# Kernel tuning notes

Measured on AMD Instinct MI355X. Metric: run time of the kernel, lower is better.

## Reference

```python
import jax, jax.numpy as jnp
import numpy as np

TAU = 0.1
K = 60.0
CHUNK = 64
B = 1024


def setup_inputs() -> dict:
    key = jax.random.key(0)
    k1, k2, k3, k4 = jax.random.split(key, 4)
    s_v = jax.random.normal(k1, (B, B), jnp.float32)
    s_l = jax.random.normal(k2, (B, B), jnp.float32)
    # class-label based positive/negative masks (typical metric-learning batch)
    labels = jax.random.randint(k3, (B,), 0, B // 8)
    pos_mask = labels[:, None] == labels[None, :]
    neg_mask = ~pos_mask
    w_v = jax.random.uniform(k4, (B, B), jnp.float32)
    w_l = 1.0 - w_v
    return dict(s_v=s_v, s_l=s_l, pos_mask=pos_mask, neg_mask=neg_mask, w_v=w_v, w_l=w_l)


def _soft_ranks(sim, pos_f, neg_f, tau=TAU, chunk=CHUNK):
    """Row-chunked differentiable soft ranks. sim/pos_f/neg_f: [B, B] float."""
    b = sim.shape[0]
    nc = b // chunk  # B divisible by chunk

    def body(args):
        cs, cp, cn = args                                   # [chunk, B] each
        # sig[c, k, j] = sigmoid((s_ck - s_cj) / tau)
        sig = jax.nn.sigmoid((cs[:, :, None] - cs[:, None, :]) / tau)
        rank_pos = 1.0 + jnp.einsum('ckj,ck->cj', sig, cn)  # count negatives above
        rank_neg = 1.0 + jnp.einsum('ckj,ck->cj', sig, cp)  # count positives above
        return rank_pos * cp + rank_neg * cn

    args = (sim.reshape(nc, chunk, b), pos_f.reshape(nc, chunk, b), neg_f.reshape(nc, chunk, b))
    return jax.lax.map(jax.checkpoint(body), args).reshape(b, b)


def reference(s_v, s_l, pos_mask, neg_mask, w_v, w_l):
    pos_f = pos_mask.astype(s_v.dtype)
    neg_f = neg_mask.astype(s_v.dtype)
    rank_v = _soft_ranks(s_v, pos_f, neg_f)
    rank_l = _soft_ranks(s_l, pos_f, neg_f)
    S_hat = (K + 1.0) * (w_v / (K + rank_v) + w_l / (K + rank_l))
    return S_hat
```

## Files before the change

### kernel.cpp

```cpp
#include <hip/hip_runtime.h>


#define NB 1024
#define CEXP 14.426950408889634f
#define SCL  0.000030517578125f
#define NBUK 128
#define BUK0 4.3f
#define BUKW 14.883720930f
#define DBUK 4
#define CHSZ 128
#define NJOB 32
#define MAXPOS 64
#define ECLMP 1e17f

typedef __attribute__((ext_vector_type(2))) float f32x2;
typedef __attribute__((ext_vector_type(2))) int   i32x2;

__device__ __forceinline__ f32x2 pk_fma(f32x2 a, f32x2 b, f32x2 c) {
    f32x2 d;
    asm("v_pk_fma_f32 %0, %1, %2, %3" : "=v"(d) : "v"(a), "v"(b), "v"(c));
    return d;
}
__device__ __forceinline__ f32x2 pk_mul(f32x2 a, f32x2 b) {
    f32x2 d;
    asm("v_pk_mul_f32 %0, %1, %2" : "=v"(d) : "v"(a), "v"(b));
    return d;
}
__device__ __forceinline__ f32x2 pk_add(f32x2 a, f32x2 b) {
    f32x2 d;
    asm("v_pk_add_f32 %0, %1, %2" : "=v"(d) : "v"(a), "v"(b));
    return d;
}
__device__ __forceinline__ f32x2 pk_fma_sat_lo(f32x2 es, f32x2 rp, f32x2 scl) {
    f32x2 d;
    asm("v_pk_fma_f32 %0, %1, %2, %3 op_sel_hi:[1,0,1] clamp"
        : "=v"(d) : "v"(es), "v"(rp), "v"(scl));
    return d;
}
__device__ __forceinline__ f32x2 pk_fma_sat_hi(f32x2 es, f32x2 rp, f32x2 scl) {
    f32x2 d;
    asm("v_pk_fma_f32 %0, %1, %2, %3 op_sel:[0,1,0] clamp"
        : "=v"(d) : "v"(es), "v"(rp), "v"(scl));
    return d;
}

#define PKTREE(L2q, Es2, A2, SCL2, TWO2, M1C)                      \
    {                                                              \
        const f32x2 P0 = (L2q)[0], P1 = (L2q)[1];                  \
        const f32x2 P2 = (L2q)[2], P3 = (L2q)[3];                  \
        const f32x2 y1 = pk_fma_sat_lo((Es2), P0, (SCL2));         \
        const f32x2 y2 = pk_fma_sat_hi((Es2), P0, (SCL2));         \
        const f32x2 y3 = pk_fma_sat_lo((Es2), P1, (SCL2));         \
        const f32x2 y4 = pk_fma_sat_hi((Es2), P1, (SCL2));         \
        const f32x2 y5 = pk_fma_sat_lo((Es2), P2, (SCL2));         \
        const f32x2 y6 = pk_fma_sat_hi((Es2), P2, (SCL2));         \
        const f32x2 y7 = pk_fma_sat_lo((Es2), P3, (SCL2));         \
        const f32x2 y8 = pk_fma_sat_hi((Es2), P3, (SCL2));         \
        const f32x2 p12 = pk_mul(y1, y2), p34 = pk_mul(y3, y4);    \
        const f32x2 p56 = pk_mul(y5, y6), p78 = pk_mul(y7, y8);    \
        const f32x2 s12 = pk_add(y1, y2), s34 = pk_add(y3, y4);    \
        const f32x2 s56 = pk_add(y5, y6), s78 = pk_add(y7, y8);    \
        const f32x2 q1 = pk_mul(p12, p34), q2 = pk_mul(p56, p78);  \
        const f32x2 n1 = pk_fma(s12, p34, pk_mul(s34, p12));       \
        const f32x2 n2 = pk_fma(s56, p78, pk_mul(s78, p56));       \
        const f32x2 num = pk_fma(n1, q2, pk_mul(n2, q1));          \
        const f32x2 den = pk_mul(q1, q2);                          \
        const i32x2 bi = 0x7EF311C3 - __builtin_bit_cast(i32x2, den); \
        f32x2 rr = __builtin_bit_cast(f32x2, bi);                  \
        const f32x2 dn = pk_mul(den, (M1C));                       \
        rr = pk_mul(rr, pk_fma(dn, rr, (TWO2)));                   \
        rr = pk_mul(rr, pk_fma(dn, rr, (TWO2)));                   \
        (A2) = pk_fma(num, rr, (A2));                              \
    }

__global__ __launch_bounds__(512) void drank_kernel(
    const float* __restrict__ s_v, const float* __restrict__ s_l,
    const unsigned char* __restrict__ pos_m,
    const unsigned char* __restrict__ neg_m,
    const float* __restrict__ w_v, const float* __restrict__ w_l,
    float* __restrict__ out)
{
    __shared__ __align__(16) float listRv[NB], listRl[NB];
    __shared__ unsigned char bktv[NB], bktl[NB];
    __shared__ unsigned short invv[NB], invl[NB];
    __shared__ float  sAv1[NB], sAv2[NB];
    __shared__ float  sAl1[NB], sAl2[NB];
    __shared__ int    offv[NBUK + 1], offl[NBUK + 1];
    __shared__ int    curv[NBUK], curl[NBUK];
    __shared__ float  SRv[129], SEv[129];
    __shared__ float  SR2v[129], SE2v[129];
    __shared__ float  SRl[129], SEl[129];
    __shared__ float  SR2l[129], SE2l[129];
    __shared__ float2 posR[MAXPOS];
    __shared__ int    npos_s, jobCtr;

    const int c = blockIdx.x;
    const int t = threadIdx.x;
    const long row = (long)c * NB;

    if (t < NBUK) { curv[t] = 0; curl[t] = 0; }
    if (t == 0) { npos_s = 0; jobCtr = 0; }
    __syncthreads();

    const unsigned int W =
        ((const unsigned int*)pos_m)[0] ^ ((const unsigned int*)neg_m)[0];
    const int mode = (W == 0x01010101u) ? 0 : ((W == 0x3f800000u) ? 2 : 1);

    const int j0 = t * 2;
    const float2 sjv = *(const float2*)(s_v + row + j0);
    const float2 sjl = *(const float2*)(s_l + row + j0);
    const float svu[2] = {sjv.x, sjv.y};
    const float slu[2] = {sjl.x, sjl.y};

    float Rv[2], Rl[2], Ev[2], El[2];
    int ibv[2], ibl[2];
    #pragma unroll
    for (int u = 0; u < 2; ++u) {
        Rv[u] = __builtin_amdgcn_exp2f(-svu[u] * CEXP);
        Rl[u] = __builtin_amdgcn_exp2f(-slu[u] * CEXP);
        Ev[u] = __builtin_amdgcn_exp2f(svu[u] * CEXP);
        El[u] = __builtin_amdgcn_exp2f(slu[u] * CEXP);
        ibv[u] = max(0, min(NBUK - 1, (int)((svu[u] + BUK0) * BUKW)));
        ibl[u] = max(0, min(NBUK - 1, (int)((slu[u] + BUK0) * BUKW)));
        atomicAdd(&curv[ibv[u]], 1);
        atomicAdd(&curl[ibl[u]], 1);
    }

    bool pj[2];
    if (mode == 0) {
        const unsigned short b = ((const unsigned short*)pos_m)[(row >> 1) + t];
        pj[0] = (b & 0x00ffu) != 0; pj[1] = (b & 0xff00u) != 0;
    } else if (mode == 2) {
        const float2 p = *(const float2*)((const float*)pos_m + row + j0);
        pj[0] = p.x != 0.f; pj[1] = p.y != 0.f;
    } else {
        const int2 p = *(const int2*)((const int*)pos_m + row + j0);
        pj[0] = p.x != 0; pj[1] = p.y != 0;
    }
    #pragma unroll
    for (int u = 0; u < 2; ++u) {
        if (pj[u]) {
            const int idx = atomicAdd(&npos_s, 1);
            if (idx < MAXPOS) posR[idx] = make_float2(Rv[u], Rl[u]);
        }
    }
    __syncthreads();

    if (t < 128) {
        const int m = t >> 6, l = t & 63;
        int* cnt = m ? curl : curv;
        int* off = m ? offl : offv;
        const int c0 = cnt[2 * l], c1 = cnt[2 * l + 1];
        int s = c0 + c1;
        #pragma unroll
        for (int d = 1; d < 64; d <<= 1) {
            const int y = __shfl_up(s, d, 64);
            if (l >= d) s += y;
        }
        const int excl = s - c0 - c1;
        off[2 * l] = excl;     off[2 * l + 1] = excl + c0;
        cnt[2 * l] = excl;     cnt[2 * l + 1] = excl + c0;
        if (l == 63) off[NBUK] = s;
    }
    __syncthreads();

    #pragma unroll
    for (int u = 0; u < 2; ++u) {
        const int pv = atomicAdd(&curv[ibv[u]], 1);
        listRv[pv] = Rv[u];
        bktv[pv]   = (unsigned char)ibv[u];
        invv[j0 + u] = (unsigned short)pv;
        const int pl = atomicAdd(&curl[ibl[u]], 1);
        listRl[pl] = Rl[u];
        bktl[pl]   = (unsigned char)ibl[u];
        invl[j0 + u] = (unsigned short)pl;
    }
    __syncthreads();

    {
        const int wid = t >> 6, l = t & 63;
        const int m   = (wid >> 1) & 1;
        const int fE  = wid & 1;
        const int sq  = wid >> 2;
        const float4* L4 = (const float4*)(m ? listRl : listRv);
        float* arr;
        switch (wid) {
            case 0: arr = SRv;  break;  case 1: arr = SEv;  break;
            case 2: arr = SRl;  break;  case 3: arr = SEl;  break;
            case 4: arr = SR2v; break;  case 5: arr = SE2v; break;
            case 6: arr = SR2l; break;  default: arr = SE2l; break;
        }
        const int o0 = fE ? (2 * l) : (127 - 2 * l);
        const int o1 = fE ? (2 * l + 1) : (126 - 2 * l);
        float s01[2];
        #pragma unroll
        for (int q = 0; q < 2; ++q) {
            const int o = q ? o1 : o0;
            const float4 a = L4[2 * o], b = L4[2 * o + 1];
            float x[8] = {a.x, a.y, a.z, a.w, b.x, b.y, b.z, b.w};
            float acc = 0.f;
            #pragma unroll
            for (int i = 0; i < 8; ++i) {
                const float v = fE ? __builtin_amdgcn_rcpf(x[i]) : x[i];
                if (sq) { const float vc = fminf(v, ECLMP); acc += vc * vc; }
                else    { acc += v; }
            }
            s01[q] = acc;
        }
        float s = s01[0] + s01[1];
        #pragma unroll
        for (int d = 1; d < 64; d <<= 1) {
            const float y = __shfl_up(s, d, 64);
            if (l >= d) s += y;
        }
        if (fE) {
            const float excl = s - s01[0] - s01[1];
            arr[o0] = excl;  arr[o1] = excl + s01[0];
            if (l == 63) arr[128] = s;
        } else {
            arr[o1] = s;  arr[o0] = s - s01[1];
            if (l == 0) arr[128] = 0.f;
        }
    }
    __syncthreads();

    static const unsigned char CORD[8] = {3, 4, 2, 5, 1, 6, 0, 7};
    const int lane = t & 63;
    const f32x2 SCL2 = {SCL, SCL};
    const f32x2 TWO2 = {2.0f, 2.0f};
    const f32x2 M1C  = {-1.0f, -1.0f};

    for (;;) {
        int jid0 = 0;
        if (lane == 0) jid0 = atomicAdd(&jobCtr, 1);
        const int jid = __builtin_amdgcn_readfirstlane(jid0);
        if (jid >= NJOB) break;
        const int ch = CORD[jid >> 2];
        const int m  = (jid >> 1) & 1;
        const int h  = jid & 1;

        const float* LR  = m ? listRl : listRv;
        const unsigned char* BK = m ? bktl : bktv;
        const int*   off = m ? offl : offv;
        float*       SA  = h ? (m ? sAl2 : sAv2) : (m ? sAl1 : sAv1);
        const float* SR  = m ? SRl : SRv;
        const float* SE  = m ? SEl : SEv;
        const float* SR2 = m ? SR2l : SR2v;
        const float* SE2 = m ? SE2l : SE2v;
        const f32x2* L2  = (const f32x2*)LR;

        const int p0 = ch * CHSZ + 2 * lane;
        const float2 R2 = *(const float2*)(LR + p0);
        const float Ex = __builtin_amdgcn_rcpf(R2.x);
        const float Ey = __builtin_amdgcn_rcpf(R2.y);
        const f32x2 Es2 = {SCL * Ex, SCL * Ey};

        const int bs = (int)BK[ch * CHSZ];
        const int be = (int)BK[ch * CHSZ + CHSZ - 1];
        const int lo0 = off[max(0, bs - DBUK)] & ~7;
        const int hi0 = (off[min(NBUK - 1, be + DBUK) + 1] + 7) & ~7;
        const int mid = ((lo0 + hi0) >> 1) & ~7;
        const int lo = h ? mid : lo0;
        const int hi = h ? hi0 : mid;

        f32x2 A2 = {0.f, 0.f};
        #pragma unroll 2
        for (int p = lo; p < hi; p += 8) {
            const f32x2* L2q = L2 + (p >> 1);
            PKTREE(L2q, Es2, A2, SCL2, TWO2, M1C);
        }
        float cx, cy;
        if (h) {
            const float sr = SR[hi0 >> 3], sr2 = SR2[hi0 >> 3];
            const float Exc = fminf(Ex, ECLMP), Eyc = fminf(Ey, ECLMP);
            cx = fmaf(Exc * Exc, sr2, (float)(NB - hi0) - Ex * sr);
            cy = fmaf(Eyc * Eyc, sr2, (float)(NB - hi0) - Ey * sr);
        } else {
            const float se = SE[lo0 >> 3], se2 = SE2[lo0 >> 3];
            const float Rxc = fminf(R2.x, ECLMP), Ryc = fminf(R2.y, ECLMP);
            cx = fmaf(-(Rxc * Rxc), se2, R2.x * se);
            cy = fmaf(-(Ryc * Ryc), se2, R2.y * se);
        }
        float2 r;
        r.x = fmaf(A2.x, SCL, cx);
        r.y = fmaf(A2.y, SCL, cy);
        *(float2*)(SA + p0) = r;
    }

    float sPv[2] = {0.f, 0.f};
    float sPl[2] = {0.f, 0.f};
    const int np = min(npos_s, MAXPOS);
    for (int i = 0; i < np; ++i) {
        const float2 rp = posR[i];
        #pragma unroll
        for (int u = 0; u < 2; ++u) {
            sPv[u] += __builtin_amdgcn_rcpf(fmaf(Ev[u], rp.x, 1.0f));
            sPl[u] += __builtin_amdgcn_rcpf(fmaf(El[u], rp.y, 1.0f));
        }
    }
    __syncthreads();

    const int iv0 = invv[j0], iv1 = invv[j0 + 1];
    const int il0 = invl[j0], il1 = invl[j0 + 1];
    const float sAvu[2] = {sAv1[iv0] + sAv2[iv0], sAv1[iv1] + sAv2[iv1]};
    const float sAlu[2] = {sAl1[il0] + sAl2[il0], sAl1[il1] + sAl2[il1]};
    const float2 wv = *(const float2*)(w_v + row + j0);
    const float2 wl = *(const float2*)(w_l + row + j0);
    const float wva[2] = {wv.x, wv.y};
    const float wla[2] = {wl.x, wl.y};
    float o[2];
    #pragma unroll
    for (int u = 0; u < 2; ++u) {
        const float rv = pj[u] ? (1.0f + sAvu[u] - sPv[u]) : (1.0f + sPv[u]);
        const float rl = pj[u] ? (1.0f + sAlu[u] - sPl[u]) : (1.0f + sPl[u]);
        o[u] = 61.0f * (wva[u] / (60.0f + rv) + wla[u] / (60.0f + rl));
    }
    float2 o2;
    o2.x = o[0]; o2.y = o[1];
    *(float2*)(out + row + j0) = o2;
}

extern "C" void kernel_launch(void* const* d_in, const int* in_sizes, int n_in,
                              void* d_out, int out_size, void* d_ws, size_t ws_size,
                              hipStream_t stream) {
    const float* s_v = (const float*)d_in[0];
    const float* s_l = (const float*)d_in[1];
    const unsigned char* pos_m = (const unsigned char*)d_in[2];
    const unsigned char* neg_m = (const unsigned char*)d_in[3];
    const float* w_v = (const float*)d_in[4];
    const float* w_l = (const float*)d_in[5];
    float* out = (float*)d_out;

    drank_kernel<<<dim3(NB), dim3(512), 0, stream>>>(s_v, s_l, pos_m, neg_m, w_v, w_l, out);
}
```

Measured before the change: 127.3 us.

## Add third-order tail series terms, narrow bucket window, drop one Newton step

Adds cubic prefix-sum tables so the far-field sigmoid tail approximation includes a third-order term. This lets the exact near-field bucket window shrink from 4 to 3 buckets, so the inner PKTREE loop runs fewer iterations. It also removes one Newton-Raphson refinement of the reciprocal in the inner loop. The cost is extra prefix-scan work (12 tables instead of 8, so some waves do two passes) and lower reciprocal precision, which adds accuracy risk.

```diff
diff --git a/kernel.cpp b/kernel.cpp
--- a/kernel.cpp
+++ b/kernel.cpp
@@ -7,11 +7,12 @@
 #define NBUK 128
 #define BUK0 4.3f
 #define BUKW 14.883720930f
-#define DBUK 4
+#define DBUK 3
 #define CHSZ 128
 #define NJOB 32
 #define MAXPOS 64
 #define ECLMP 1e17f
+#define CLMP3 3e11f
 
 typedef __attribute__((ext_vector_type(2))) float f32x2;
 typedef __attribute__((ext_vector_type(2))) int   i32x2;
@@ -69,7 +70,6 @@
         f32x2 rr = __builtin_bit_cast(f32x2, bi);                  \
         const f32x2 dn = pk_mul(den, (M1C));                       \
         rr = pk_mul(rr, pk_fma(dn, rr, (TWO2)));                   \
-        rr = pk_mul(rr, pk_fma(dn, rr, (TWO2)));                   \
         (A2) = pk_fma(num, rr, (A2));                              \
     }
 
@@ -91,6 +91,8 @@
     __shared__ float  SR2v[129], SE2v[129];
     __shared__ float  SRl[129], SEl[129];
     __shared__ float  SR2l[129], SE2l[129];
+    __shared__ float  SR3v[129], SE3v[129];
+    __shared__ float  SR3l[129], SE3l[129];
     __shared__ float2 posR[MAXPOS];
     __shared__ int    npos_s, jobCtr;
 
@@ -179,47 +181,56 @@
 
     {
         const int wid = t >> 6, l = t & 63;
-        const int m   = (wid >> 1) & 1;
-        const int fE  = wid & 1;
-        const int sq  = wid >> 2;
-        const float4* L4 = (const float4*)(m ? listRl : listRv);
-        float* arr;
-        switch (wid) {
-            case 0: arr = SRv;  break;  case 1: arr = SEv;  break;
-            case 2: arr = SRl;  break;  case 3: arr = SEl;  break;
-            case 4: arr = SR2v; break;  case 5: arr = SE2v; break;
-            case 6: arr = SR2l; break;  default: arr = SE2l; break;
-        }
-        const int o0 = fE ? (2 * l) : (127 - 2 * l);
-        const int o1 = fE ? (2 * l + 1) : (126 - 2 * l);
-        float s01[2];
-        #pragma unroll
-        for (int q = 0; q < 2; ++q) {
-            const int o = q ? o1 : o0;
-            const float4 a = L4[2 * o], b = L4[2 * o + 1];
-            float x[8] = {a.x, a.y, a.z, a.w, b.x, b.y, b.z, b.w};
-            float acc = 0.f;
+        for (int f = wid; f < 12; f += 8) {
+            const int m   = (f >> 1) & 1;
+            const int fE  = f & 1;
+            const int pw  = f >> 2;
+            const float4* L4 = (const float4*)(m ? listRl : listRv);
+            float* arr;
+            switch (f) {
+                case 0:  arr = SRv;  break;  case 1:  arr = SEv;  break;
+                case 2:  arr = SRl;  break;  case 3:  arr = SEl;  break;
+                case 4:  arr = SR2v; break;  case 5:  arr = SE2v; break;
+                case 6:  arr = SR2l; break;  case 7:  arr = SE2l; break;
+                case 8:  arr = SR3v; break;  case 9:  arr = SE3v; break;
+                case 10: arr = SR3l; break;  default: arr = SE3l; break;
+            }
+            const int o0 = fE ? (2 * l) : (127 - 2 * l);
+            const int o1 = fE ? (2 * l + 1) : (126 - 2 * l);
+            float s01[2];
             #pragma unroll
-            for (int i = 0; i < 8; ++i) {
-                const float v = fE ? __builtin_amdgcn_rcpf(x[i]) : x[i];
-                if (sq) { const float vc = fminf(v, ECLMP); acc += vc * vc; }
-                else    { acc += v; }
+            for (int q = 0; q < 2; ++q) {
+                const int o = q ? o1 : o0;
+                const float4 a = L4[2 * o], b = L4[2 * o + 1];
+                float x[8] = {a.x, a.y, a.z, a.w, b.x, b.y, b.z, b.w};
+                float acc = 0.f;
+                #pragma unroll
+                for (int i = 0; i < 8; ++i) {
+                    const float v = fE ? __builtin_amdgcn_rcpf(x[i]) : x[i];
+                    if (pw == 1) {
+                        const float vc = fminf(v, ECLMP); acc += vc * vc;
+                    } else if (pw == 2) {
+                        const float vc = fminf(v, CLMP3); acc += vc * vc * vc;
+                    } else {
+                        acc += v;
+                    }
+                }
+                s01[q] = acc;
             }
-            s01[q] = acc;
-        }
-        float s = s01[0] + s01[1];
-        #pragma unroll
-        for (int d = 1; d < 64; d <<= 1) {
-            const float y = __shfl_up(s, d, 64);
-            if (l >= d) s += y;
-        }
-        if (fE) {
-            const float excl = s - s01[0] - s01[1];
-            arr[o0] = excl;  arr[o1] = excl + s01[0];
-            if (l == 63) arr[128] = s;
-        } else {
-            arr[o1] = s;  arr[o0] = s - s01[1];
-            if (l == 0) arr[128] = 0.f;
+            float s = s01[0] + s01[1];
+            #pragma unroll
+            for (int d = 1; d < 64; d <<= 1) {
+                const float y = __shfl_up(s, d, 64);
+                if (l >= d) s += y;
+            }
+            if (fE) {
+                const float excl = s - s01[0] - s01[1];
+                arr[o0] = excl;  arr[o1] = excl + s01[0];
+                if (l == 63) arr[128] = s;
+            } else {
+                arr[o1] = s;  arr[o0] = s - s01[1];
+                if (l == 0) arr[128] = 0.f;
+            }
         }
     }
     __syncthreads();
@@ -247,6 +258,8 @@
         const float* SE  = m ? SEl : SEv;
         const float* SR2 = m ? SR2l : SR2v;
         const float* SE2 = m ? SE2l : SE2v;
+        const float* SR3 = m ? SR3l : SR3v;
+        const float* SE3 = m ? SE3l : SE3v;
         const f32x2* L2  = (const f32x2*)LR;
 
         const int p0 = ch * CHSZ + 2 * lane;
@@ -271,15 +284,21 @@
         }
         float cx, cy;
         if (h) {
-            const float sr = SR[hi0 >> 3], sr2 = SR2[hi0 >> 3];
+            const float sr = SR[hi0 >> 3], sr2 = SR2[hi0 >> 3], sr3 = SR3[hi0 >> 3];
             const float Exc = fminf(Ex, ECLMP), Eyc = fminf(Ey, ECLMP);
-            cx = fmaf(Exc * Exc, sr2, (float)(NB - hi0) - Ex * sr);
-            cy = fmaf(Eyc * Eyc, sr2, (float)(NB - hi0) - Ey * sr);
+            const float Ex3 = fminf(Ex, CLMP3), Ey3 = fminf(Ey, CLMP3);
+            cx = fmaf(Exc * Exc, sr2, (float)(NB - hi0) - Ex * sr)
+                 - (Ex3 * Ex3 * Ex3) * sr3;
+            cy = fmaf(Eyc * Eyc, sr2, (float)(NB - hi0) - Ey * sr)
+                 - (Ey3 * Ey3 * Ey3) * sr3;
         } else {
-            const float se = SE[lo0 >> 3], se2 = SE2[lo0 >> 3];
+            const float se = SE[lo0 >> 3], se2 = SE2[lo0 >> 3], se3 = SE3[lo0 >> 3];
             const float Rxc = fminf(R2.x, ECLMP), Ryc = fminf(R2.y, ECLMP);
-            cx = fmaf(-(Rxc * Rxc), se2, R2.x * se);
-            cy = fmaf(-(Ryc * Ryc), se2, R2.y * se);
+            const float Rx3 = fminf(R2.x, CLMP3), Ry3 = fminf(R2.y, CLMP3);
+            cx = fmaf(-(Rxc * Rxc), se2, R2.x * se)
+                 + (Rx3 * Rx3 * Rx3) * se3;
+            cy = fmaf(-(Ryc * Ryc), se2, R2.y * se)
+                 + (Ry3 * Ry3 * Ry3) * se3;
         }
         float2 r;
         r.x = fmaf(A2.x, SCL, cx);
```

Result: faster. 122.5 us (-3.8%).
